# Kernel optimization log

Measured on AMD Instinct MI355X. Metric: run time of the kernel, lower is better.

Reference implementation:

```python
import jax, jax.numpy as jnp
import numpy as np

DIM = 128
NUM_HEADS = 4
WH, WW = 7, 7
N = WH * WW
B_ = 4096


def _relative_position_index():
    coords_h = np.arange(WH)
    coords_w = np.arange(WW)
    coords = np.stack(np.meshgrid(coords_h, coords_w, indexing='ij'))  # (2, Wh, Ww)
    coords_flat = coords.reshape(2, -1)  # (2, N)
    rel = coords_flat[:, :, None] - coords_flat[:, None, :]  # (2, N, N)
    rel = rel.transpose(1, 2, 0).astype(np.int32)  # (N, N, 2)
    rel[:, :, 0] += WH - 1
    rel[:, :, 1] += WW - 1
    rel[:, :, 0] *= 2 * WW - 1
    return rel.sum(-1)  # (N, N) int32


def setup_inputs() -> dict:
    key = jax.random.key(0)
    ks = jax.random.split(key, 6)
    x = jax.random.normal(ks[0], (B_, N, DIM), dtype=jnp.float32)
    # torch nn.Linear-style params: weight (out, in), bias (out,)
    qkv_w = jax.random.normal(ks[1], (3 * DIM, DIM), dtype=jnp.float32) * (DIM ** -0.5)
    qkv_b = jnp.zeros((3 * DIM,), dtype=jnp.float32)
    proj_w = jax.random.normal(ks[2], (DIM, DIM), dtype=jnp.float32) * (DIM ** -0.5)
    proj_b = jnp.zeros((DIM,), dtype=jnp.float32)
    rpb_table = jax.random.normal(ks[3], ((2 * WH - 1) * (2 * WW - 1), NUM_HEADS), dtype=jnp.float32) * 0.02
    rpi = jnp.asarray(_relative_position_index())  # (N, N) int32
    return {"x": x, "qkv_w": qkv_w, "qkv_b": qkv_b, "proj_w": proj_w,
            "proj_b": proj_b, "rpb_table": rpb_table, "rpi": rpi}


def reference(x, qkv_w, qkv_b, proj_w, proj_b, rpb_table, rpi):
    b, n, c = x.shape
    h = NUM_HEADS
    hd = c // h
    scale = hd ** -0.5
    qkv = jnp.einsum('bnc,oc->bno', x, qkv_w) + qkv_b  # (B_, N, 3C)
    qkv = qkv.reshape(b, n, 3, h, hd)
    q = jnp.transpose(qkv[:, :, 0], (0, 2, 1, 3))  # (b, h, n, hd)
    k = jnp.transpose(qkv[:, :, 1], (0, 2, 1, 3))
    v = jnp.transpose(qkv[:, :, 2], (0, 2, 1, 3))
    attn = jnp.einsum('bhnd,bhmd->bhnm', q * scale, k)  # (b, h, n, n)
    bias = rpb_table[rpi.reshape(-1)].reshape(n, n, h)  # gather bias per pair
    attn = attn + jnp.transpose(bias, (2, 0, 1))[None]  # (1, h, n, n)
    attn = jax.nn.softmax(attn, axis=-1)
    out = jnp.einsum('bhnm,bhmd->bhnd', attn, v)
    out = jnp.transpose(out, (0, 2, 1, 3)).reshape(b, n, c)
    out = jnp.einsum('bnc,oc->bno', out, proj_w) + proj_b
    return out
```

## Files before the change

kernel.cpp:

```cpp
#include <hip/hip_runtime.h>
#include <hip/hip_bf16.h>

typedef __attribute__((ext_vector_type(8))) short s16x8;
typedef __attribute__((ext_vector_type(4))) float f32x4;
typedef unsigned short u16;

#define NTOK 49
#define CDIM 128
#define NWIN 4096
#define LOG2E 1.4426950408889634f
#define SCL (0.17677669529663687f * LOG2E)

#define XT_STRIDE 136
#define HEAD_SZ 4096
#define K_OFF 2048
#define LDS_ELEMS 16384

__device__ __forceinline__ u16 f2bf(float f) {
    __hip_bfloat16 h = __float2bfloat16(f);
    return __builtin_bit_cast(u16, h);
}
__device__ __forceinline__ unsigned pk2(float a, float b) {
    return (unsigned)f2bf(a) | ((unsigned)f2bf(b) << 16);
}

__global__ void prep_kernel(const float* __restrict__ qkv_w,
                            const float* __restrict__ proj_w,
                            const float* __restrict__ rpb,
                            const int* __restrict__ rpi,
                            const float* __restrict__ qkv_b,
                            u16* __restrict__ pkq, u16* __restrict__ pkp,
                            float* __restrict__ bMv, float* __restrict__ bias2) {
    int idx = blockIdx.x * blockDim.x + threadIdx.x;
    if (idx < 49152) {
        int r = idx & 7, lane = (idx >> 3) & 63, tile = idx >> 9;
        int ot = tile % 24, kt = tile / 24;
        int o = ot * 16 + (lane & 15);
        int k = kt * 32 + ((lane >> 4) << 3) + r;
        float w = qkv_w[o * CDIM + k];
        if (o < 128) w *= SCL;
        pkq[idx] = f2bf(w);
    } else if (idx < 65536) {
        int i2 = idx - 49152;
        int r = i2 & 7, lane = (i2 >> 3) & 63, tile = i2 >> 9;
        int ot = tile & 7, kt = tile >> 3;
        int o = ot * 16 + (lane & 15);
        int k = kt * 32 + ((lane >> 4) << 3) + r;
        pkp[i2] = f2bf(proj_w[o * CDIM + k]);
    } else if (idx < 81920) {
        int i = idx - 65536;
        int r = i & 3, lr = (i >> 2) & 15, g = (i >> 6) & 3;
        int nt = (i >> 8) & 3, mt = (i >> 10) & 3, h = i >> 12;
        int q = nt * 16 + lr, j = mt * 16 + 4 * g + r;
        bMv[i] = (q < NTOK && j < NTOK) ? rpb[rpi[q * NTOK + j] * 4 + h] * LOG2E : -1e30f;
    } else if (idx < 82304) {
        int o = idx - 81920;
        bias2[o] = qkv_b[o] * (o < 128 ? SCL : 1.0f);
    }
}

__global__ __launch_bounds__(256, 4) void winattn_kernel(
    const float* __restrict__ x, const float* __restrict__ bias2,
    const float* __restrict__ proj_b,
    const u16* __restrict__ pkq, const u16* __restrict__ pkp,
    const float* __restrict__ bMv, float* __restrict__ out) {
    __shared__ __align__(16) u16 smem[LDS_ELEMS];
    const int b = blockIdx.x;
    const int tid = threadIdx.x;
    const int wave = tid >> 6, lane = tid & 63;
    const int g = lane >> 4, lr = lane & 15;
    const int qs = ((lr >> 1) & 3) << 3;

    u16* xt = smem;

    const float* xp = x + (size_t)b * (NTOK * CDIM);
    float4 xin[7];
#pragma unroll
    for (int u = 0; u < 6; ++u)
        xin[u] = reinterpret_cast<const float4*>(xp)[tid + u * 256];
    if (tid < 32) xin[6] = reinterpret_cast<const float4*>(xp)[1536 + tid];
#pragma unroll
    for (int u = 0; u < 6; ++u) {
        int lin = (tid + u * 256) * 4;
        int i = lin >> 7, c = lin & 127;
        uint2 pkv;
        pkv.x = pk2(xin[u].x, xin[u].y);
        pkv.y = pk2(xin[u].z, xin[u].w);
        *reinterpret_cast<uint2*>(&xt[i * XT_STRIDE + c]) = pkv;
    }
    if (tid < 32) {
        int lin = (1536 + tid) * 4;
        int i = lin >> 7, c = lin & 127;
        uint2 pkv;
        pkv.x = pk2(xin[6].x, xin[6].y);
        pkv.y = pk2(xin[6].z, xin[6].w);
        *reinterpret_cast<uint2*>(&xt[i * XT_STRIDE + c]) = pkv;
    }
    {
        const uint2 z2 = {0u, 0u};
#pragma unroll
        for (int u = 0; u < 2; ++u)
            *reinterpret_cast<uint2*>(&xt[NTOK * XT_STRIDE + (tid + u * 256) * 4]) = z2;
    }
    __syncthreads();

    const s16x8* pkqv = reinterpret_cast<const s16x8*>(pkq);

    f32x4 acc_v[4][2];
#pragma unroll
    for (int t1 = 0; t1 < 2; ++t1) {
        float vb = bias2[256 + (2 * wave + t1) * 16 + lr];
#pragma unroll
        for (int mt = 0; mt < 4; ++mt) acc_v[mt][t1] = (f32x4){vb, vb, vb, vb};
    }
#pragma unroll
    for (int kt = 0; kt < 4; ++kt) {
        s16x8 af[4];
#pragma unroll
        for (int tt = 0; tt < 4; ++tt)
            af[tt] = *reinterpret_cast<const s16x8*>(&xt[(tt * 16 + lr) * XT_STRIDE + kt * 32 + g * 8]);
        s16x8 wv[2];
#pragma unroll
        for (int t1 = 0; t1 < 2; ++t1)
            wv[t1] = pkqv[(kt * 24 + 16 + 2 * wave + t1) * 64 + lane];
        __builtin_amdgcn_s_setprio(1);
#pragma unroll
        for (int mt = 0; mt < 4; ++mt)
#pragma unroll
            for (int t1 = 0; t1 < 2; ++t1)
                acc_v[mt][t1] = __builtin_amdgcn_mfma_f32_16x16x32_bf16(af[mt], wv[t1], acc_v[mt][t1], 0, 0, 0);
        __builtin_amdgcn_s_setprio(0);
    }
    unsigned vpk[4][2][2];
#pragma unroll
    for (int t1 = 0; t1 < 2; ++t1)
#pragma unroll
        for (int mt = 0; mt < 4; ++mt) {
            vpk[mt][t1][0] = pk2(acc_v[mt][t1][0], acc_v[mt][t1][1]);
            vpk[mt][t1][1] = pk2(acc_v[mt][t1][2], acc_v[mt][t1][3]);
        }

    f32x4 acc_qk[4][4];
#pragma unroll
    for (int t = 0; t < 4; ++t) {
        f32x4 b4 = *reinterpret_cast<const f32x4*>(bias2 + (t >> 1) * 128 + (2 * wave + (t & 1)) * 16 + 4 * g);
#pragma unroll
        for (int tt = 0; tt < 4; ++tt) acc_qk[t][tt] = b4;
    }
#pragma unroll
    for (int kt = 0; kt < 4; ++kt) {
        s16x8 af[4];
#pragma unroll
        for (int tt = 0; tt < 4; ++tt)
            af[tt] = *reinterpret_cast<const s16x8*>(&xt[(tt * 16 + lr) * XT_STRIDE + kt * 32 + g * 8]);
        s16x8 wq[4];
#pragma unroll
        for (int t = 0; t < 4; ++t) {
            int ot = (t >> 1) * 8 + 2 * wave + (t & 1);
            wq[t] = pkqv[(kt * 24 + ot) * 64 + lane];
        }
        __builtin_amdgcn_s_setprio(1);
#pragma unroll
        for (int t = 0; t < 4; ++t)
#pragma unroll
            for (int tt = 0; tt < 4; ++tt)
                acc_qk[t][tt] = __builtin_amdgcn_mfma_f32_16x16x32_bf16(wq[t], af[tt], acc_qk[t][tt], 0, 0, 0);
        __builtin_amdgcn_s_setprio(0);
    }
    __syncthreads();

    u16* hb = smem + wave * HEAD_SZ;
    u16* qb = hb;
    u16* kb = hb + K_OFF;
#pragma unroll
    for (int t = 0; t < 4; ++t) {
        u16* base = (t < 2) ? qb : kb;
        int c0 = (16 * (t & 1) + 4 * g) ^ qs;
#pragma unroll
        for (int tt = 0; tt < 4; ++tt) {
            uint2 w2;
            w2.x = pk2(acc_qk[t][tt][0], acc_qk[t][tt][1]);
            w2.y = pk2(acc_qk[t][tt][2], acc_qk[t][tt][3]);
            *reinterpret_cast<uint2*>(&base[(tt * 16 + lr) * 32 + c0]) = w2;
        }
    }
    asm volatile("s_waitcnt lgkmcnt(0)" ::: "memory");

    const f32x4* bv4 = reinterpret_cast<const f32x4*>(bMv);
    f32x4 st[4][4];
    {
        s16x8 ak[4], bq[4];
        int rc = (g * 8) ^ qs;
#pragma unroll
        for (int mt = 0; mt < 4; ++mt)
            ak[mt] = *reinterpret_cast<const s16x8*>(&kb[(mt * 16 + lr) * 32 + rc]);
#pragma unroll
        for (int nt = 0; nt < 4; ++nt)
            bq[nt] = *reinterpret_cast<const s16x8*>(&qb[(nt * 16 + lr) * 32 + rc]);
        __builtin_amdgcn_s_setprio(1);
#pragma unroll
        for (int mt = 0; mt < 4; ++mt)
#pragma unroll
            for (int nt = 0; nt < 4; ++nt)
                st[mt][nt] = __builtin_amdgcn_mfma_f32_16x16x32_bf16(
                    ak[mt], bq[nt], bv4[(((wave * 4 + mt) * 4 + nt) * 4 + g) * 16 + lr], 0, 0, 0);
        __builtin_amdgcn_s_setprio(0);
    }
    float inv[4];
#pragma unroll
    for (int nt = 0; nt < 4; ++nt) {
        float s = 0.f;
#pragma unroll
        for (int mt = 0; mt < 4; ++mt)
#pragma unroll
            for (int r = 0; r < 4; ++r) {
                float e = exp2f(st[mt][nt][r]);
                st[mt][nt][r] = e;
                s += e;
            }
        s += __shfl_xor(s, 16, 64);
        s += __shfl_xor(s, 32, 64);
        inv[nt] = 1.0f / s;
    }
    char* pB = reinterpret_cast<char*>(hb);
#pragma unroll
    for (int mt = 0; mt < 4; ++mt)
#pragma unroll
        for (int nt = 0; nt < 4; ++nt) {
            uint2 w2;
            w2.x = pk2(st[mt][nt][0], st[mt][nt][1]);
            w2.y = pk2(st[mt][nt][2], st[mt][nt][3]);
            int q = nt * 16 + lr;
            int off = (q * 128 + mt * 32 + g * 8) ^ ((q & 7) << 4);
            *reinterpret_cast<uint2*>(pB + off) = w2;
        }
    asm volatile("s_waitcnt lgkmcnt(0)" ::: "memory");

    const int srcA4 = (((lane & 16) << 1) | lr) << 2;
    const int srcB4 = srcA4 + 64;
    const bool hi32 = (lane & 32) != 0;
    f32x4 ov[2][4] = {};
    {
        s16x8 va[2][2], pbf[4][2];
#pragma unroll
        for (int t1 = 0; t1 < 2; ++t1)
#pragma unroll
            for (int kk = 0; kk < 2; ++kk) {
                union { s16x8 v; unsigned u[4]; } tmp;
#pragma unroll
                for (int w = 0; w < 4; ++w) {
                    int src = (w < 2) ? srcA4 : srcB4;
                    unsigned lo = (unsigned)__builtin_amdgcn_ds_bpermute(src, (int)vpk[2 * kk][t1][w & 1]);
                    unsigned hh = (unsigned)__builtin_amdgcn_ds_bpermute(src, (int)vpk[2 * kk + 1][t1][w & 1]);
                    tmp.u[w] = hi32 ? hh : lo;
                }
                va[t1][kk] = tmp.v;
            }
#pragma unroll
        for (int nt = 0; nt < 4; ++nt)
#pragma unroll
            for (int kk = 0; kk < 2; ++kk) {
                int off = (((nt * 16 + lr) * 128) + kk * 64 + g * 16) ^ ((lr & 7) << 4);
                pbf[nt][kk] = *reinterpret_cast<const s16x8*>(pB + off);
            }
        __builtin_amdgcn_s_setprio(1);
#pragma unroll
        for (int t1 = 0; t1 < 2; ++t1)
#pragma unroll
            for (int nt = 0; nt < 4; ++nt)
#pragma unroll
                for (int kk = 0; kk < 2; ++kk)
                    ov[t1][nt] = __builtin_amdgcn_mfma_f32_16x16x32_bf16(va[t1][kk], pbf[nt][kk], ov[t1][nt], 0, 0, 0);
        __builtin_amdgcn_s_setprio(0);
    }
#pragma unroll
    for (int t1 = 0; t1 < 2; ++t1)
#pragma unroll
        for (int nt = 0; nt < 4; ++nt)
#pragma unroll
            for (int r = 0; r < 4; ++r) ov[t1][nt][r] *= inv[nt];

    s16x8 pfr[4][2];
    const s16x8* pkpv = reinterpret_cast<const s16x8*>(pkp);
#pragma unroll
    for (int kt = 0; kt < 4; ++kt)
#pragma unroll
        for (int t = 0; t < 2; ++t)
            pfr[kt][t] = pkpv[(kt * 8 + 2 * wave + t) * 64 + lane];

#pragma unroll
    for (int t1 = 0; t1 < 2; ++t1)
#pragma unroll
        for (int nt = 0; nt < 4; ++nt) {
            uint2 w2;
            w2.x = pk2(ov[t1][nt][0], ov[t1][nt][1]);
            w2.y = pk2(ov[t1][nt][2], ov[t1][nt][3]);
            int lg = 2 * t1 + (g >> 1);
            int off = (nt * 16 + lr) * 32 + (((lg << 3) ^ qs)) + ((g & 1) << 2);
            *reinterpret_cast<uint2*>(&hb[off]) = w2;
        }
    __syncthreads();

    f32x4 pacc[2][4];
#pragma unroll
    for (int t = 0; t < 2; ++t) {
        f32x4 pb4 = *reinterpret_cast<const f32x4*>(proj_b + (2 * wave + t) * 16 + 4 * g);
#pragma unroll
        for (int tt = 0; tt < 4; ++tt) pacc[t][tt] = pb4;
    }
#pragma unroll
    for (int kt = 0; kt < 4; ++kt) {
        s16x8 af2[4];
#pragma unroll
        for (int tt = 0; tt < 4; ++tt)
            af2[tt] = *reinterpret_cast<const s16x8*>(&smem[kt * HEAD_SZ + (tt * 16 + lr) * 32 + ((g * 8) ^ qs)]);
        __builtin_amdgcn_s_setprio(1);
#pragma unroll
        for (int t = 0; t < 2; ++t)
#pragma unroll
            for (int tt = 0; tt < 4; ++tt)
                pacc[t][tt] = __builtin_amdgcn_mfma_f32_16x16x32_bf16(pfr[kt][t], af2[tt], pacc[t][tt], 0, 0, 0);
        __builtin_amdgcn_s_setprio(0);
    }
    float* outp = out + (size_t)b * (NTOK * CDIM);
#pragma unroll
    for (int tt = 0; tt < 4; ++tt) {
        int tok = tt * 16 + lr;
        if (tok < NTOK) {
#pragma unroll
            for (int t = 0; t < 2; ++t) {
                int oc0 = (2 * wave + t) * 16 + 4 * g;
                *reinterpret_cast<f32x4*>(outp + (size_t)tok * CDIM + oc0) = pacc[t][tt];
            }
        }
    }
}

extern "C" void kernel_launch(void* const* d_in, const int* in_sizes, int n_in,
                              void* d_out, int out_size, void* d_ws, size_t ws_size,
                              hipStream_t stream) {
    const float* x      = (const float*)d_in[0];
    const float* qkv_w  = (const float*)d_in[1];
    const float* qkv_b  = (const float*)d_in[2];
    const float* proj_w = (const float*)d_in[3];
    const float* proj_b = (const float*)d_in[4];
    const float* rpb    = (const float*)d_in[5];
    const int*   rpi    = (const int*)d_in[6];
    float* out = (float*)d_out;

    u16*   pkq   = (u16*)d_ws;
    u16*   pkp   = pkq + 49152;
    float* bMv   = (float*)((char*)d_ws + 131072);
    float* bias2 = (float*)((char*)d_ws + 196608);

    prep_kernel<<<322, 256, 0, stream>>>(qkv_w, proj_w, rpb, rpi, qkv_b, pkq, pkp, bMv, bias2);
    winattn_kernel<<<NWIN, 256, 0, stream>>>(x, bias2, proj_b, pkq, pkp, bMv, out);
}
```

Measured before the change: 83.84 us.

## Process two windows per block and prefetch next window's input during attention

Each block now handles two consecutive windows. The global loads of the second window's x are issued in the middle of the first window's compute, after the softmax writes, so their latency overlaps the PV and projection MFMAs. The grid is halved to 2048 blocks. This raises register pressure by 28 extra floats held live across the first body, which could cause spills or lower occupancy. Fewer blocks may also reduce the latency hiding that came from having many independent blocks in flight.

```diff
diff --git a/kernel.cpp b/kernel.cpp
--- a/kernel.cpp
+++ b/kernel.cpp
@@ -59,26 +59,7 @@
     }
 }
 
-__global__ __launch_bounds__(256, 4) void winattn_kernel(
-    const float* __restrict__ x, const float* __restrict__ bias2,
-    const float* __restrict__ proj_b,
-    const u16* __restrict__ pkq, const u16* __restrict__ pkp,
-    const float* __restrict__ bMv, float* __restrict__ out) {
-    __shared__ __align__(16) u16 smem[LDS_ELEMS];
-    const int b = blockIdx.x;
-    const int tid = threadIdx.x;
-    const int wave = tid >> 6, lane = tid & 63;
-    const int g = lane >> 4, lr = lane & 15;
-    const int qs = ((lr >> 1) & 3) << 3;
-
-    u16* xt = smem;
-
-    const float* xp = x + (size_t)b * (NTOK * CDIM);
-    float4 xin[7];
-#pragma unroll
-    for (int u = 0; u < 6; ++u)
-        xin[u] = reinterpret_cast<const float4*>(xp)[tid + u * 256];
-    if (tid < 32) xin[6] = reinterpret_cast<const float4*>(xp)[1536 + tid];
+__device__ __forceinline__ void xt_write(u16* __restrict__ xt, const float4* xin, int tid) {
 #pragma unroll
     for (int u = 0; u < 6; ++u) {
         int lin = (tid + u * 256) * 4;
@@ -96,15 +77,20 @@
         pkv.y = pk2(xin[6].z, xin[6].w);
         *reinterpret_cast<uint2*>(&xt[i * XT_STRIDE + c]) = pkv;
     }
-    {
-        const uint2 z2 = {0u, 0u};
-#pragma unroll
-        for (int u = 0; u < 2; ++u)
-            *reinterpret_cast<uint2*>(&xt[NTOK * XT_STRIDE + (tid + u * 256) * 4]) = z2;
-    }
-    __syncthreads();
-
-    const s16x8* pkqv = reinterpret_cast<const s16x8*>(pkq);
+    const uint2 z2 = {0u, 0u};
+#pragma unroll
+    for (int u = 0; u < 2; ++u)
+        *reinterpret_cast<uint2*>(&xt[NTOK * XT_STRIDE + (tid + u * 256) * 4]) = z2;
+}
+
+__device__ __forceinline__ void win_body(
+    u16* __restrict__ smem, float* __restrict__ outp,
+    const float* __restrict__ bias2, const float* __restrict__ proj_b,
+    const s16x8* __restrict__ pkqv, const s16x8* __restrict__ pkpv,
+    const f32x4* __restrict__ bv4,
+    const float* __restrict__ xpN, float4* xinN, bool issueNext,
+    int wave, int lane, int g, int lr, int qs, int tid) {
+    u16* xt = smem;
 
     f32x4 acc_v[4][2];
 #pragma unroll
@@ -186,7 +172,6 @@
     }
     asm volatile("s_waitcnt lgkmcnt(0)" ::: "memory");
 
-    const f32x4* bv4 = reinterpret_cast<const f32x4*>(bMv);
     f32x4 st[4][4];
     {
         s16x8 ak[4], bq[4];
@@ -234,6 +219,13 @@
             int off = (q * 128 + mt * 32 + g * 8) ^ ((q & 7) << 4);
             *reinterpret_cast<uint2*>(pB + off) = w2;
         }
+
+    if (issueNext) {
+#pragma unroll
+        for (int u = 0; u < 6; ++u)
+            xinN[u] = reinterpret_cast<const float4*>(xpN)[tid + u * 256];
+        if (tid < 32) xinN[6] = reinterpret_cast<const float4*>(xpN)[1536 + tid];
+    }
     asm volatile("s_waitcnt lgkmcnt(0)" ::: "memory");
 
     const int srcA4 = (((lane & 16) << 1) | lr) << 2;
@@ -281,7 +273,6 @@
             for (int r = 0; r < 4; ++r) ov[t1][nt][r] *= inv[nt];
 
     s16x8 pfr[4][2];
-    const s16x8* pkpv = reinterpret_cast<const s16x8*>(pkp);
 #pragma unroll
     for (int kt = 0; kt < 4; ++kt)
 #pragma unroll
@@ -322,7 +313,6 @@
                 pacc[t][tt] = __builtin_amdgcn_mfma_f32_16x16x32_bf16(pfr[kt][t], af2[tt], pacc[t][tt], 0, 0, 0);
         __builtin_amdgcn_s_setprio(0);
     }
-    float* outp = out + (size_t)b * (NTOK * CDIM);
 #pragma unroll
     for (int tt = 0; tt < 4; ++tt) {
         int tok = tt * 16 + lr;
@@ -334,6 +324,49 @@
             }
         }
     }
+}
+
+__global__ __launch_bounds__(256, 4) void winattn_kernel(
+    const float* __restrict__ x, const float* __restrict__ bias2,
+    const float* __restrict__ proj_b,
+    const u16* __restrict__ pkq, const u16* __restrict__ pkp,
+    const float* __restrict__ bMv, float* __restrict__ out) {
+    __shared__ __align__(16) u16 smem[LDS_ELEMS];
+    const int tid = threadIdx.x;
+    const int wave = tid >> 6, lane = tid & 63;
+    const int g = lane >> 4, lr = lane & 15;
+    const int qs = ((lr >> 1) & 3) << 3;
+
+    const s16x8* pkqv = reinterpret_cast<const s16x8*>(pkq);
+    const s16x8* pkpv = reinterpret_cast<const s16x8*>(pkp);
+    const f32x4* bv4 = reinterpret_cast<const f32x4*>(bMv);
+
+    const int b0 = blockIdx.x * 2;
+    const float* xpA = x + (size_t)b0 * (NTOK * CDIM);
+    const float* xpB = xpA + NTOK * CDIM;
+    float* outA = out + (size_t)b0 * (NTOK * CDIM);
+    float* outB = outA + NTOK * CDIM;
+
+    {
+        float4 xinA[7];
+#pragma unroll
+        for (int u = 0; u < 6; ++u)
+            xinA[u] = reinterpret_cast<const float4*>(xpA)[tid + u * 256];
+        if (tid < 32) xinA[6] = reinterpret_cast<const float4*>(xpA)[1536 + tid];
+        xt_write(smem, xinA, tid);
+    }
+    __syncthreads();
+
+    float4 xinB[7];
+    win_body(smem, outA, bias2, proj_b, pkqv, pkpv, bv4,
+             xpB, xinB, true, wave, lane, g, lr, qs, tid);
+
+    __syncthreads();
+    xt_write(smem, xinB, tid);
+    __syncthreads();
+
+    win_body(smem, outB, bias2, proj_b, pkqv, pkpv, bv4,
+             nullptr, nullptr, false, wave, lane, g, lr, qs, tid);
 }
 
 extern "C" void kernel_launch(void* const* d_in, const int* in_sizes, int n_in,
@@ -354,5 +387,5 @@
     float* bias2 = (float*)((char*)d_ws + 196608);
 
     prep_kernel<<<322, 256, 0, stream>>>(qkv_w, proj_w, rpb, rpi, qkv_b, pkq, pkp, bMv, bias2);
-    winattn_kernel<<<NWIN, 256, 0, stream>>>(x, bias2, proj_b, pkq, pkp, bMv, out);
-}
+    winattn_kernel<<<NWIN / 2, 256, 0, stream>>>(x, bias2, proj_b, pkq, pkp, bMv, out);
+}
```

Result: slower. 206.5 us (+146.3%).
